# Optimization experiments

Hardware: AMD Instinct MI355X
Metric: run time of the kernel (lower is better)

Reference implementation:

```python
import jax, jax.numpy as jnp
import numpy as np

B, CIN, COUT, H, W, KS, PAD = 8, 64, 128, 32, 32, 3, 1
OH, OW = H, W  # stride 1, pad 1, dilation 1 -> same spatial size
QMIN, QMAX = -128, 127


def setup_inputs() -> dict:
    key = jax.random.key(0)
    k1, k2, k3 = jax.random.split(key, 3)
    x = jax.random.normal(k1, (B, CIN, H, W), jnp.float32)
    weight = jax.random.normal(k2, (COUT, CIN, KS, KS), jnp.float32) * 0.05
    bias = jax.random.normal(k3, (COUT,), jnp.float32) * 0.01
    # exact int8 product LUT: lut[a+128, b+128] = a*b (the 'approximate multiplier' table)
    q = jnp.arange(QMIN, QMAX + 1, dtype=jnp.int32)  # [256]
    lut = q[:, None] * q[None, :]                     # [256,256] int32
    # gradient LUT: d(a*b)/da = b, d(a*b)/db = a
    gradient_lut = jnp.stack([
        jnp.broadcast_to(q[None, :], (256, 256)),
        jnp.broadcast_to(q[:, None], (256, 256)),
    ]).astype(jnp.float32)                            # [2,256,256]
    T_feature = jnp.ones((1,), jnp.float32)
    T_weight = jnp.ones((1,), jnp.float32)
    return {"x": x, "weight": weight, "bias": bias, "lut": lut,
            "gradient_lut": gradient_lut, "T_feature": T_feature, "T_weight": T_weight}


def _quantize(v, T):
    scale = 127.0 / T
    return jnp.clip(jnp.round(v * scale), QMIN, QMAX).astype(jnp.int32)


def _lut_conv(xq, wq, lut):
    """LUT-based int8 conv. xq [B,CIN,H,W] int32 in [-128,127], wq [COUT,CIN,KS,KS]."""
    xp = jnp.pad(xq, ((0, 0), (0, 0), (PAD, PAD), (PAD, PAD)))
    # im2col: 9 structurally-distinct kernel offsets (fixed small loop)
    patches = jnp.stack([xp[:, :, i:i + OH, j:j + OW]
                         for i in range(KS) for j in range(KS)], axis=2)  # [B,CIN,9,OH,OW]
    K = CIN * KS * KS
    cols = patches.transpose(0, 3, 4, 1, 2).reshape(B * OH * OW, K)  # [P,K]
    wf = wq.reshape(COUT, K)                                         # [COUT,K]
    lut_flat = lut.reshape(-1)

    def step(acc, xs):
        xk, wk = xs  # xk [P], wk [COUT]
        idx = (xk[:, None] + 128) * 256 + (wk[None, :] + 128)  # [P,COUT]
        return acc + lut_flat[idx], None

    acc0 = jnp.zeros((B * OH * OW, COUT), jnp.int32)
    acc, _ = jax.lax.scan(step, acc0, (cols.T, wf.T))  # scan over K patch elems
    return acc.reshape(B, OH, OW, COUT).transpose(0, 3, 1, 2)  # [B,COUT,OH,OW]


def reference(x, weight, bias, lut, gradient_lut, T_feature, T_weight):
    # EMA threshold update (update_T_func), detached scalars in the original
    Tf = 0.95 * T_feature[0] + 0.05 * jnp.max(jnp.abs(x))
    Tw = 0.95 * T_weight[0] + 0.05 * jnp.max(jnp.abs(weight))
    xq = _quantize(x, Tf)
    wq = _quantize(weight, Tw)
    acc = _lut_conv(xq, wq, lut).astype(jnp.float32)
    out = acc * ((Tf / 127.0) * (Tw / 127.0)) + bias[None, :, None, None]
    return out
```

## Files before the change

### kernel.cpp

```cpp
#include <hip/hip_runtime.h>
#include <cstdint>

#define BATCH 8
#define CIN 64
#define COUT 128
#define HH 32
#define WW 32
#define PH 34
#define PW 34

typedef int v4i __attribute__((ext_vector_type(4)));

#define WS_TF 0
#define WS_TW 1
#define WS_PART 16
#define XPAD_OFF 4096
#define WFRAG_OFF (4096 + BATCH * PH * PW * CIN)

__global__ __launch_bounds__(256) void absmax_partial(const float* __restrict__ x,
                                                      const float* __restrict__ w,
                                                      float* __restrict__ partials) {
    float m = 0.0f;
    if (blockIdx.x < 128) {
        const float4* p = (const float4*)x;
        int base = blockIdx.x * 1024 + threadIdx.x;
        #pragma unroll
        for (int k = 0; k < 4; ++k) {
            float4 v = p[base + k * 256];
            m = fmaxf(m, fmaxf(fmaxf(fabsf(v.x), fabsf(v.y)), fmaxf(fabsf(v.z), fabsf(v.w))));
        }
    } else {
        const float4* p = (const float4*)w;
        int wb = blockIdx.x - 128;
        int base = wb * 1152 + threadIdx.x;
        int end = (wb + 1) * 1152;
        #pragma unroll
        for (int k = 0; k < 5; ++k) {
            int i = base + k * 256;
            if (i < end) {
                float4 v = p[i];
                m = fmaxf(m, fmaxf(fmaxf(fabsf(v.x), fabsf(v.y)), fmaxf(fabsf(v.z), fabsf(v.w))));
            }
        }
    }
    #pragma unroll
    for (int off = 32; off > 0; off >>= 1)
        m = fmaxf(m, __shfl_xor(m, off, 64));
    __shared__ float sm[4];
    int wave = threadIdx.x >> 6;
    if ((threadIdx.x & 63) == 0) sm[wave] = m;
    __syncthreads();
    if (threadIdx.x == 0)
        partials[WS_PART + blockIdx.x] = fmaxf(fmaxf(sm[0], sm[1]), fmaxf(sm[2], sm[3]));
}

__device__ __forceinline__ unsigned quantb(float v, float scale) {
    float q = rintf(v * scale);
    q = fminf(fmaxf(q, -128.0f), 127.0f);
    return ((unsigned)(int)q) & 255u;
}

#define QB_X 256
#define QB_W 72
#define QB_Z 66
__global__ __launch_bounds__(256) void quant_pack(const float* __restrict__ x,
                                                  const float* __restrict__ w,
                                                  const float* __restrict__ Tf_in,
                                                  const float* __restrict__ Tw_in,
                                                  float* __restrict__ ws_f32,
                                                  uint8_t* __restrict__ xpad,
                                                  uint8_t* __restrict__ wfrag) {
    int blk = blockIdx.x;
    int t = threadIdx.x;
    int lane = t & 63;

    if (blk < QB_X) {
        float m = fmaxf(ws_f32[WS_PART + lane], ws_f32[WS_PART + 64 + lane]);
        #pragma unroll
        for (int off = 32; off > 0; off >>= 1)
            m = fmaxf(m, __shfl_xor(m, off, 64));
        float a = 0.95f * Tf_in[0];
        float bt = 0.05f * m;
        float Tf = a + bt;
        if (blk == 0 && t == 0) ws_f32[WS_TF] = Tf;
        float scale = 127.0f / Tf;

        int b = blk >> 5, h = blk & 31;
        const float4* x4 = (const float4*)x;
        __shared__ unsigned lds[CIN * 9];
        #pragma unroll
        for (int k = 0; k < 2; ++k) {
            int f = t + k * 256;
            int ci = f >> 3, wq = f & 7;
            float4 v = x4[(b * CIN + ci) * 256 + h * 8 + wq];
            unsigned pack = quantb(v.x, scale) | (quantb(v.y, scale) << 8) |
                            (quantb(v.z, scale) << 16) | (quantb(v.w, scale) << 24);
            lds[ci * 9 + wq] = pack;
        }
        __syncthreads();
        const uint8_t* ldsb = (const uint8_t*)lds;
        unsigned* orow = (unsigned*)(xpad + (((b * PH) + (h + 1)) * PW + 1) * CIN);
        #pragma unroll
        for (int k = 0; k < 2; ++k) {
            int o = t + k * 256;
            int ww_ = o >> 4, c4 = o & 15;
            unsigned d = (unsigned)ldsb[(c4 * 4 + 0) * 36 + ww_]
                       | ((unsigned)ldsb[(c4 * 4 + 1) * 36 + ww_] << 8)
                       | ((unsigned)ldsb[(c4 * 4 + 2) * 36 + ww_] << 16)
                       | ((unsigned)ldsb[(c4 * 4 + 3) * 36 + ww_] << 24);
            orow[o] = d;
        }
    } else if (blk < QB_X + QB_W) {
        float m = ws_f32[WS_PART + 128 + (lane & 15)];
        #pragma unroll
        for (int off = 32; off > 0; off >>= 1)
            m = fmaxf(m, __shfl_xor(m, off, 64));
        float a = 0.95f * Tw_in[0];
        float bt = 0.05f * m;
        float Tw = a + bt;
        if (blk == QB_X && t == 0) ws_f32[WS_TW] = Tw;
        float scale = 127.0f / Tw;

        int tid = (blk - QB_X) * 256 + t;
        int idx4 = tid * 4;
        int j0 = idx4 & 15;
        int ln = (idx4 >> 4) & 63;
        int f  = idx4 >> 10;
        int g = f & 7;
        int tap = f >> 3;
        int kh = tap / 3, kw = tap - kh * 3;
        int co = g * 16 + (ln & 15);
        int ci0 = (ln >> 4) * 16 + j0;
        unsigned pack = 0;
        #pragma unroll
        for (int c = 0; c < 4; ++c) {
            float v = w[((co * CIN + ci0 + c) * 3 + kh) * 3 + kw];
            pack |= quantb(v, scale) << (8 * c);
        }
        ((unsigned*)wfrag)[tid] = pack;
    } else {
        int j = (blk - QB_X - QB_W) * 256 + t;
        int p = j >> 4, c4 = j & 15;
        int b = p / 132;
        int r = p - b * 132;
        int ih, iw;
        if (r < 34)      { ih = 0;          iw = r; }
        else if (r < 68) { ih = PH - 1;     iw = r - 34; }
        else if (r < 100){ ih = r - 68 + 1; iw = 0; }
        else             { ih = r - 100 + 1; iw = PW - 1; }
        ((unsigned*)xpad)[((b * PH + ih) * PW + iw) * 16 + c4] = 0u;
    }
}

__global__ __launch_bounds__(256, 2) void conv_mfma(const uint8_t* __restrict__ xpad,
                                                    const uint8_t* __restrict__ wfrag,
                                                    const float* __restrict__ bias,
                                                    const float* __restrict__ ws_f32,
                                                    float* __restrict__ out) {
    int blk = blockIdx.x;
    int nb = blk & 1;
    int mb = blk >> 1;
    int b = mb >> 5;
    int oh = mb & 31;
    int wave = threadIdx.x >> 6;
    int lane = threadIdx.x & 63;
    int mt = wave & 1;
    int nh2 = wave >> 1;
    int row = lane & 15;
    int quad = lane >> 4;

    v4i acc[2];
    acc[0] = (v4i){0, 0, 0, 0};
    acc[1] = (v4i){0, 0, 0, 0};

    const uint8_t* xbase = xpad + (((b * PH + oh) * PW) + mt * 16 + row) * CIN + quad * 16;

    #pragma unroll
    for (int tp = 0; tp < 9; ++tp) {
        const int kh = tp / 3, kw = tp % 3;
        v4i afrag = *(const v4i*)(xbase + (kh * PW + kw) * CIN);
        #pragma unroll
        for (int nt = 0; nt < 2; ++nt) {
            int g = nb * 4 + nh2 * 2 + nt;
            v4i bfrag = *(const v4i*)(wfrag + (((tp * 8 + g) * 64) + lane) * 16);
            acc[nt] = __builtin_amdgcn_mfma_i32_16x16x64_i8(afrag, bfrag, acc[nt], 0, 0, 0);
        }
    }

    float Tf = ws_f32[WS_TF];
    float Tw = ws_f32[WS_TW];
    float s = (Tf / 127.0f) * (Tw / 127.0f);
    int ow0 = mt * 16 + quad * 4;
    #pragma unroll
    for (int nt = 0; nt < 2; ++nt) {
        int g = nb * 4 + nh2 * 2 + nt;
        int co = g * 16 + row;
        float bb = bias[co];
        float4 o;
        o.x = (float)acc[nt][0] * s + bb;
        o.y = (float)acc[nt][1] * s + bb;
        o.z = (float)acc[nt][2] * s + bb;
        o.w = (float)acc[nt][3] * s + bb;
        *(float4*)(out + (((b * COUT + co) * HH + oh) * WW) + ow0) = o;
    }
}

extern "C" void kernel_launch(void* const* d_in, const int* in_sizes, int n_in,
                              void* d_out, int out_size, void* d_ws, size_t ws_size,
                              hipStream_t stream) {
    const float* x        = (const float*)d_in[0];
    const float* weight   = (const float*)d_in[1];
    const float* bias     = (const float*)d_in[2];
    const float* T_feature = (const float*)d_in[5];
    const float* T_weight  = (const float*)d_in[6];

    float*   ws_f32 = (float*)d_ws;
    uint8_t* xpad   = (uint8_t*)d_ws + XPAD_OFF;
    uint8_t* wfrag  = (uint8_t*)d_ws + WFRAG_OFF;

    absmax_partial<<<144, 256, 0, stream>>>(x, weight, ws_f32);
    quant_pack<<<QB_X + QB_W + QB_Z, 256, 0, stream>>>(x, weight, T_feature, T_weight,
                                                       ws_f32, xpad, wfrag);
    conv_mfma<<<512, 256, 0, stream>>>(xpad, wfrag, bias, ws_f32, (float*)d_out);
}
```

Before: 75.00 us.

## Fuse absmax, quantize-pack and MFMA conv into one cooperative kernel

Replaces the three separate launches (absmax reduction, quantize/pack, conv) with one cooperative kernel of 512 blocks that uses grid-wide syncs between phases. Each block first reduces a slice of x and w to per-block maxima. After a grid sync, every block redundantly finishes the reduction to get Tf and Tw locally, so no scalar round-trip through memory is needed before the conv. The goal is to remove launch gaps and inter-kernel drain; the cost is two grid barriers and the requirement that all 512 blocks be co-resident.

```diff
diff --git a/kernel.cpp b/kernel.cpp
--- a/kernel.cpp
+++ b/kernel.cpp
@@ -1,5 +1,8 @@
 #include <hip/hip_runtime.h>
+#include <hip/hip_cooperative_groups.h>
 #include <cstdint>
+
+namespace cg = cooperative_groups;
 
 #define BATCH 8
 #define CIN 64
@@ -11,48 +14,14 @@
 
 typedef int v4i __attribute__((ext_vector_type(4)));
 
-#define WS_TF 0
-#define WS_TW 1
-#define WS_PART 16
+#define WS_PX 0
+#define WS_PW 512
 #define XPAD_OFF 4096
 #define WFRAG_OFF (4096 + BATCH * PH * PW * CIN)
 
-__global__ __launch_bounds__(256) void absmax_partial(const float* __restrict__ x,
-                                                      const float* __restrict__ w,
-                                                      float* __restrict__ partials) {
-    float m = 0.0f;
-    if (blockIdx.x < 128) {
-        const float4* p = (const float4*)x;
-        int base = blockIdx.x * 1024 + threadIdx.x;
-        #pragma unroll
-        for (int k = 0; k < 4; ++k) {
-            float4 v = p[base + k * 256];
-            m = fmaxf(m, fmaxf(fmaxf(fabsf(v.x), fabsf(v.y)), fmaxf(fabsf(v.z), fabsf(v.w))));
-        }
-    } else {
-        const float4* p = (const float4*)w;
-        int wb = blockIdx.x - 128;
-        int base = wb * 1152 + threadIdx.x;
-        int end = (wb + 1) * 1152;
-        #pragma unroll
-        for (int k = 0; k < 5; ++k) {
-            int i = base + k * 256;
-            if (i < end) {
-                float4 v = p[i];
-                m = fmaxf(m, fmaxf(fmaxf(fabsf(v.x), fabsf(v.y)), fmaxf(fabsf(v.z), fabsf(v.w))));
-            }
-        }
-    }
-    #pragma unroll
-    for (int off = 32; off > 0; off >>= 1)
-        m = fmaxf(m, __shfl_xor(m, off, 64));
-    __shared__ float sm[4];
-    int wave = threadIdx.x >> 6;
-    if ((threadIdx.x & 63) == 0) sm[wave] = m;
-    __syncthreads();
-    if (threadIdx.x == 0)
-        partials[WS_PART + blockIdx.x] = fmaxf(fmaxf(sm[0], sm[1]), fmaxf(sm[2], sm[3]));
-}
+#define QB_X 256
+#define QB_W 72
+#define QB_Z 66
 
 __device__ __forceinline__ unsigned quantb(float v, float scale) {
     float q = rintf(v * scale);
@@ -60,34 +29,75 @@
     return ((unsigned)(int)q) & 255u;
 }
 
-#define QB_X 256
-#define QB_W 72
-#define QB_Z 66
-__global__ __launch_bounds__(256) void quant_pack(const float* __restrict__ x,
-                                                  const float* __restrict__ w,
-                                                  const float* __restrict__ Tf_in,
-                                                  const float* __restrict__ Tw_in,
-                                                  float* __restrict__ ws_f32,
-                                                  uint8_t* __restrict__ xpad,
-                                                  uint8_t* __restrict__ wfrag) {
-    int blk = blockIdx.x;
-    int t = threadIdx.x;
-    int lane = t & 63;
+__global__ __launch_bounds__(256, 2) void fused_all(const float* __restrict__ x,
+                                                    const float* __restrict__ w,
+                                                    const float* __restrict__ bias,
+                                                    const float* __restrict__ Tf_in,
+                                                    const float* __restrict__ Tw_in,
+                                                    float* __restrict__ ws_f32,
+                                                    uint8_t* __restrict__ xpad,
+                                                    uint8_t* __restrict__ wfrag,
+                                                    float* __restrict__ out) {
+    cg::grid_group grid = cg::this_grid();
+    const int blk = blockIdx.x;
+    const int t = threadIdx.x;
+    const int lane = t & 63;
+    const int wave = t >> 6;
+
+    __shared__ float sm[8];
+    __shared__ unsigned lds[CIN * 9];
+
+    {
+        const int tid = blk * 256 + t;
+        float4 v = ((const float4*)x)[tid];
+        float mx = fmaxf(fmaxf(fabsf(v.x), fabsf(v.y)), fmaxf(fabsf(v.z), fabsf(v.w)));
+        float mw = 0.0f;
+        if (tid < 18432) {
+            float4 u = ((const float4*)w)[tid];
+            mw = fmaxf(fmaxf(fabsf(u.x), fabsf(u.y)), fmaxf(fabsf(u.z), fabsf(u.w)));
+        }
+        #pragma unroll
+        for (int off = 32; off > 0; off >>= 1) {
+            mx = fmaxf(mx, __shfl_xor(mx, off, 64));
+            mw = fmaxf(mw, __shfl_xor(mw, off, 64));
+        }
+        if (lane == 0) { sm[wave] = mx; sm[4 + wave] = mw; }
+        __syncthreads();
+        if (t == 0) {
+            ws_f32[WS_PX + blk] = fmaxf(fmaxf(sm[0], sm[1]), fmaxf(sm[2], sm[3]));
+            if (blk < 72)
+                ws_f32[WS_PW + blk] = fmaxf(fmaxf(sm[4], sm[5]), fmaxf(sm[6], sm[7]));
+        }
+        __threadfence();
+    }
+    grid.sync();
+
+    float Tf, Tw;
+    {
+        float mx = fmaxf(ws_f32[WS_PX + t], ws_f32[WS_PX + 256 + t]);
+        float mw = (t < 72) ? ws_f32[WS_PW + t] : 0.0f;
+        #pragma unroll
+        for (int off = 32; off > 0; off >>= 1) {
+            mx = fmaxf(mx, __shfl_xor(mx, off, 64));
+            mw = fmaxf(mw, __shfl_xor(mw, off, 64));
+        }
+        __syncthreads();
+        if (lane == 0) { sm[wave] = mx; sm[4 + wave] = mw; }
+        __syncthreads();
+        mx = fmaxf(fmaxf(sm[0], sm[1]), fmaxf(sm[2], sm[3]));
+        mw = fmaxf(fmaxf(sm[4], sm[5]), fmaxf(sm[6], sm[7]));
+        float af = 0.95f * Tf_in[0];
+        float bf = 0.05f * mx;
+        Tf = af + bf;
+        float aw = 0.95f * Tw_in[0];
+        float bw = 0.05f * mw;
+        Tw = aw + bw;
+    }
 
     if (blk < QB_X) {
-        float m = fmaxf(ws_f32[WS_PART + lane], ws_f32[WS_PART + 64 + lane]);
-        #pragma unroll
-        for (int off = 32; off > 0; off >>= 1)
-            m = fmaxf(m, __shfl_xor(m, off, 64));
-        float a = 0.95f * Tf_in[0];
-        float bt = 0.05f * m;
-        float Tf = a + bt;
-        if (blk == 0 && t == 0) ws_f32[WS_TF] = Tf;
         float scale = 127.0f / Tf;
-
         int b = blk >> 5, h = blk & 31;
         const float4* x4 = (const float4*)x;
-        __shared__ unsigned lds[CIN * 9];
         #pragma unroll
         for (int k = 0; k < 2; ++k) {
             int f = t + k * 256;
@@ -111,16 +121,7 @@
             orow[o] = d;
         }
     } else if (blk < QB_X + QB_W) {
-        float m = ws_f32[WS_PART + 128 + (lane & 15)];
-        #pragma unroll
-        for (int off = 32; off > 0; off >>= 1)
-            m = fmaxf(m, __shfl_xor(m, off, 64));
-        float a = 0.95f * Tw_in[0];
-        float bt = 0.05f * m;
-        float Tw = a + bt;
-        if (blk == QB_X && t == 0) ws_f32[WS_TW] = Tw;
         float scale = 127.0f / Tw;
-
         int tid = (blk - QB_X) * 256 + t;
         int idx4 = tid * 4;
         int j0 = idx4 & 15;
@@ -138,88 +139,83 @@
             pack |= quantb(v, scale) << (8 * c);
         }
         ((unsigned*)wfrag)[tid] = pack;
-    } else {
+    } else if (blk < QB_X + QB_W + QB_Z) {
         int j = (blk - QB_X - QB_W) * 256 + t;
         int p = j >> 4, c4 = j & 15;
         int b = p / 132;
         int r = p - b * 132;
         int ih, iw;
-        if (r < 34)      { ih = 0;          iw = r; }
-        else if (r < 68) { ih = PH - 1;     iw = r - 34; }
-        else if (r < 100){ ih = r - 68 + 1; iw = 0; }
+        if (r < 34)      { ih = 0;           iw = r; }
+        else if (r < 68) { ih = PH - 1;      iw = r - 34; }
+        else if (r < 100){ ih = r - 68 + 1;  iw = 0; }
         else             { ih = r - 100 + 1; iw = PW - 1; }
         ((unsigned*)xpad)[((b * PH + ih) * PW + iw) * 16 + c4] = 0u;
     }
-}
-
-__global__ __launch_bounds__(256, 2) void conv_mfma(const uint8_t* __restrict__ xpad,
-                                                    const uint8_t* __restrict__ wfrag,
-                                                    const float* __restrict__ bias,
-                                                    const float* __restrict__ ws_f32,
-                                                    float* __restrict__ out) {
-    int blk = blockIdx.x;
-    int nb = blk & 1;
-    int mb = blk >> 1;
-    int b = mb >> 5;
-    int oh = mb & 31;
-    int wave = threadIdx.x >> 6;
-    int lane = threadIdx.x & 63;
-    int mt = wave & 1;
-    int nh2 = wave >> 1;
-    int row = lane & 15;
-    int quad = lane >> 4;
-
-    v4i acc[2];
-    acc[0] = (v4i){0, 0, 0, 0};
-    acc[1] = (v4i){0, 0, 0, 0};
-
-    const uint8_t* xbase = xpad + (((b * PH + oh) * PW) + mt * 16 + row) * CIN + quad * 16;
-
-    #pragma unroll
-    for (int tp = 0; tp < 9; ++tp) {
-        const int kh = tp / 3, kw = tp % 3;
-        v4i afrag = *(const v4i*)(xbase + (kh * PW + kw) * CIN);
+    __threadfence();
+    grid.sync();
+
+    {
+        int nb = blk & 1;
+        int mb = blk >> 1;
+        int b = mb >> 5;
+        int oh = mb & 31;
+        int mt = wave & 1;
+        int nh2 = wave >> 1;
+        int row = lane & 15;
+        int quad = lane >> 4;
+
+        v4i acc[2];
+        acc[0] = (v4i){0, 0, 0, 0};
+        acc[1] = (v4i){0, 0, 0, 0};
+
+        const uint8_t* xbase = xpad + (((b * PH + oh) * PW) + mt * 16 + row) * CIN + quad * 16;
+
+        #pragma unroll
+        for (int tp = 0; tp < 9; ++tp) {
+            const int kh = tp / 3, kw = tp % 3;
+            v4i afrag = *(const v4i*)(xbase + (kh * PW + kw) * CIN);
+            #pragma unroll
+            for (int nt = 0; nt < 2; ++nt) {
+                int g = nb * 4 + nh2 * 2 + nt;
+                v4i bfrag = *(const v4i*)(wfrag + (((tp * 8 + g) * 64) + lane) * 16);
+                acc[nt] = __builtin_amdgcn_mfma_i32_16x16x64_i8(afrag, bfrag, acc[nt], 0, 0, 0);
+            }
+        }
+
+        float s = (Tf / 127.0f) * (Tw / 127.0f);
+        int ow0 = mt * 16 + quad * 4;
         #pragma unroll
         for (int nt = 0; nt < 2; ++nt) {
             int g = nb * 4 + nh2 * 2 + nt;
-            v4i bfrag = *(const v4i*)(wfrag + (((tp * 8 + g) * 64) + lane) * 16);
-            acc[nt] = __builtin_amdgcn_mfma_i32_16x16x64_i8(afrag, bfrag, acc[nt], 0, 0, 0);
-        }
-    }
-
-    float Tf = ws_f32[WS_TF];
-    float Tw = ws_f32[WS_TW];
-    float s = (Tf / 127.0f) * (Tw / 127.0f);
-    int ow0 = mt * 16 + quad * 4;
-    #pragma unroll
-    for (int nt = 0; nt < 2; ++nt) {
-        int g = nb * 4 + nh2 * 2 + nt;
-        int co = g * 16 + row;
-        float bb = bias[co];
-        float4 o;
-        o.x = (float)acc[nt][0] * s + bb;
-        o.y = (float)acc[nt][1] * s + bb;
-        o.z = (float)acc[nt][2] * s + bb;
-        o.w = (float)acc[nt][3] * s + bb;
-        *(float4*)(out + (((b * COUT + co) * HH + oh) * WW) + ow0) = o;
+            int co = g * 16 + row;
+            float bb = bias[co];
+            float4 o;
+            o.x = (float)acc[nt][0] * s + bb;
+            o.y = (float)acc[nt][1] * s + bb;
+            o.z = (float)acc[nt][2] * s + bb;
+            o.w = (float)acc[nt][3] * s + bb;
+            *(float4*)(out + (((b * COUT + co) * HH + oh) * WW) + ow0) = o;
+        }
     }
 }
 
 extern "C" void kernel_launch(void* const* d_in, const int* in_sizes, int n_in,
                               void* d_out, int out_size, void* d_ws, size_t ws_size,
                               hipStream_t stream) {
-    const float* x        = (const float*)d_in[0];
-    const float* weight   = (const float*)d_in[1];
-    const float* bias     = (const float*)d_in[2];
+    const float* x         = (const float*)d_in[0];
+    const float* weight    = (const float*)d_in[1];
+    const float* bias      = (const float*)d_in[2];
     const float* T_feature = (const float*)d_in[5];
     const float* T_weight  = (const float*)d_in[6];
 
     float*   ws_f32 = (float*)d_ws;
     uint8_t* xpad   = (uint8_t*)d_ws + XPAD_OFF;
     uint8_t* wfrag  = (uint8_t*)d_ws + WFRAG_OFF;
-
-    absmax_partial<<<144, 256, 0, stream>>>(x, weight, ws_f32);
-    quant_pack<<<QB_X + QB_W + QB_Z, 256, 0, stream>>>(x, weight, T_feature, T_weight,
-                                                       ws_f32, xpad, wfrag);
-    conv_mfma<<<512, 256, 0, stream>>>(xpad, wfrag, bias, ws_f32, (float*)d_out);
+    float*   outp   = (float*)d_out;
+
+    void* args[] = {(void*)&x, (void*)&weight, (void*)&bias, (void*)&T_feature,
+                    (void*)&T_weight, (void*)&ws_f32, (void*)&xpad, (void*)&wfrag,
+                    (void*)&outp};
+    hipLaunchCooperativeKernel((const void*)fused_all, dim3(512), dim3(256),
+                               args, 0, stream);
 }
```

After: 237.4 us. 217% more time.
